# Kernel optimization log

Hardware: AMD Instinct MI355X
Metric: run time of the kernel (lower is better)

Reference implementation:

```python
import jax, jax.numpy as jnp
import numpy as np

B, T, F, H, L, C = 32, 512, 1024, 1024, 2, 2
W_SCALE = 0.03  # small init so tanh stays in its linear-ish range


def setup_inputs() -> dict:
    key = jax.random.key(0)
    ks = jax.random.split(key, 12)
    inp = {
        "x": jax.random.normal(ks[0], (B, T, F), dtype=jnp.float32),
        "h0": jax.random.normal(ks[1], (L, B, H), dtype=jnp.float32),
        # layer 0 (input size F)
        "W_ih0": jax.random.normal(ks[2], (H, F), dtype=jnp.float32) * W_SCALE,
        "W_hh0": jax.random.normal(ks[3], (H, H), dtype=jnp.float32) * W_SCALE,
        "b_ih0": jax.random.normal(ks[4], (H,), dtype=jnp.float32) * W_SCALE,
        "b_hh0": jax.random.normal(ks[5], (H,), dtype=jnp.float32) * W_SCALE,
        # layer 1 (input size H)
        "W_ih1": jax.random.normal(ks[6], (H, H), dtype=jnp.float32) * W_SCALE,
        "W_hh1": jax.random.normal(ks[7], (H, H), dtype=jnp.float32) * W_SCALE,
        "b_ih1": jax.random.normal(ks[8], (H,), dtype=jnp.float32) * W_SCALE,
        "b_hh1": jax.random.normal(ks[9], (H,), dtype=jnp.float32) * W_SCALE,
        # classifier Linear(T*H -> C)
        "W_cls": jax.random.normal(ks[10], (C, T * H), dtype=jnp.float32) * 0.001,
        "b_cls": jax.random.normal(ks[11], (C,), dtype=jnp.float32) * 0.001,
    }
    return inp


def _rnn_layer(x_btf, h0_bh, W_ih, W_hh, b_ih, b_hh):
    # PyTorch RNN (tanh): h_t = tanh(x_t W_ih^T + b_ih + h_{t-1} W_hh^T + b_hh)
    # Precompute the input projection for all timesteps (one big GEMM).
    pre = jnp.einsum("btf,hf->bth", x_btf, W_ih) + b_ih + b_hh  # [B,T,H]
    pre_t = jnp.swapaxes(pre, 0, 1)  # [T,B,H] for scan

    def step(h, p):  # h: [B,H], p: [B,H]
        h_new = jnp.tanh(p + h @ W_hh.T)
        return h_new, h_new

    h_last, ys = jax.lax.scan(step, h0_bh, pre_t)
    return jnp.swapaxes(ys, 0, 1), h_last  # [B,T,H], [B,H]


def reference(x, h0, W_ih0, W_hh0, b_ih0, b_hh0, W_ih1, W_hh1, b_ih1, b_hh1, W_cls, b_cls):
    y0, h0_last = _rnn_layer(x, h0[0], W_ih0, W_hh0, b_ih0, b_hh0)
    y1, h1_last = _rnn_layer(y0, h0[1], W_ih1, W_hh1, b_ih1, b_hh1)
    h_n = jnp.stack([h0_last, h1_last], axis=0)  # [L,B,H]
    flat = y1.reshape(y1.shape[0], -1)  # [B, T*H]
    logits = flat @ W_cls.T + b_cls  # Dropout(0.1) is identity at inference
    return logits, h_n
```

## Files before the change

kernel.cpp:

```cpp
#include <hip/hip_runtime.h>
#include <math.h>

typedef float f4 __attribute__((ext_vector_type(4)));
typedef short bf16x8 __attribute__((ext_vector_type(8)));
typedef unsigned u32x2 __attribute__((ext_vector_type(2)));
typedef unsigned u32x4 __attribute__((ext_vector_type(4)));

#define NT 512

#define H0R 0
#define H1R 131072
#define PLOG 196608
#define FLAGS 200704
#define WSW 204800
#define XBF 4399104

__device__ __forceinline__ unsigned pack_bf16(float lo, float hi) {
  unsigned u;
  asm volatile("v_cvt_pk_bf16_f32 %0, %1, %2" : "=v"(u) : "v"(lo), "v"(hi));
  return u;
}
__device__ __forceinline__ float bflo(unsigned d) { return __uint_as_float(d << 16); }
__device__ __forceinline__ float bfhi(unsigned d) { return __uint_as_float(d & 0xffff0000u); }
__device__ __forceinline__ void st_cohf(float* p, float v) {
  __hip_atomic_store(p, v, __ATOMIC_RELAXED, __HIP_MEMORY_SCOPE_AGENT);
}
__device__ __forceinline__ void st_cohu(unsigned* p, unsigned v) {
  __hip_atomic_store(p, v, __ATOMIC_RELAXED, __HIP_MEMORY_SCOPE_AGENT);
}
__device__ __forceinline__ int ld_flag(const unsigned* p) {
  return (int)__hip_atomic_load(p, __ATOMIC_RELAXED, __HIP_MEMORY_SCOPE_AGENT);
}

__device__ __forceinline__ void split8(const f4 v0, const f4 v1, u32x4& hi, u32x4& lo) {
  float h_[8] = {v0[0], v0[1], v0[2], v0[3], v1[0], v1[1], v1[2], v1[3]};
  #pragma unroll
  for (int e = 0; e < 4; ++e) hi[e] = pack_bf16(h_[2*e], h_[2*e+1]);
  float r[8];
  #pragma unroll
  for (int e = 0; e < 4; ++e) {
    r[2*e]   = h_[2*e]   - bflo(hi[e]);
    r[2*e+1] = h_[2*e+1] - bfhi(hi[e]);
  }
  #pragma unroll
  for (int e = 0; e < 4; ++e) lo[e] = pack_bf16(r[2*e], r[2*e+1]);
}

__global__ __launch_bounds__(128) void wconv_kernel(
    const float* __restrict__ W0, const float* __restrict__ W1,
    const float* __restrict__ W2, const float* __restrict__ W3,
    float* __restrict__ ws) {
  const int mat = blockIdx.x >> 10;
  const int j = blockIdx.x & 1023;
  const int kc = threadIdx.x;
  const float* Wm = (mat == 0) ? W0 : (mat == 1) ? W1 : (mat == 2) ? W2 : W3;
  const f4* src = (const f4*)(Wm + (size_t)j * 1024 + kc * 8);
  f4 v0 = src[0], v1 = src[1];
  u32x4 hi, lo;
  split8(v0, v1, hi, lo);
  u32x4* dst = (u32x4*)((f4*)ws + (WSW >> 2));
  size_t base = (size_t)(mat * 2) * 131072 + (j >> 4) * 2048 + kc * 16 + (j & 15);
  dst[base] = hi;
  dst[base + 131072] = lo;
}

__global__ __launch_bounds__(128) void xconv_kernel(const float* __restrict__ x,
                                                    float* __restrict__ ws) {
  const int t = blockIdx.x;
  const int kc = threadIdx.x;
  u32x4* dst = (u32x4*)((f4*)ws + (XBF >> 2)) + (size_t)t * 4096;
  for (int b = 0; b < 32; ++b) {
    const f4* src = (const f4*)(x + ((size_t)b * NT + t) * 1024 + kc * 8);
    f4 v0 = src[0], v1 = src[1];
    u32x4 p;
    #pragma unroll
    for (int e = 0; e < 4; ++e)
      p[e] = pack_bf16(e < 2 ? v0[2*e] : v1[2*e-4], e < 2 ? v0[2*e+1] : v1[2*e-3]);
    dst[(size_t)kc * 32 + b] = p;
  }
}

__global__ __launch_bounds__(256) void hinit_kernel(const float* __restrict__ h0,
                                                    float* __restrict__ ws) {
  int g = blockIdx.x * 256 + threadIdx.x;
  int l = g >> 12, b = (g >> 7) & 31, kc = g & 127;
  const f4* src = (const f4*)(h0 + (size_t)l * 32768 + b * 1024 + kc * 8);
  f4 v0 = src[0], v1 = src[1];
  u32x4 hi, lo;
  split8(v0, v1, hi, lo);
  unsigned base = l ? (H1R + 32768) : (H0R + 3 * 32768);
  u32x4* d = (u32x4*)((unsigned*)ws + base);
  d[(size_t)kc * 32 + b] = hi;
  d[4096 + (size_t)kc * 32 + b] = lo;
  if (g < 4096) ((unsigned*)ws)[FLAGS + g] = 0u;
}

#define LDG(dst, ptr) \
  asm volatile("global_load_dwordx4 %0, %1, off sc0" : "=v"(dst) : "v"(ptr))
#define MFMA(a, b, c) __builtin_amdgcn_mfma_f32_16x16x32_bf16(a, b, c, 0, 0, 0)
#define BC(v) __builtin_bit_cast(bf16x8, v)

#define KT_M(kt, N)                                                       \
  asm volatile("s_waitcnt vmcnt(" #N ")");                                \
  __builtin_amdgcn_sched_barrier(0xF4);                                   \
  {                                                                       \
    const int ci = (ch0 + kt * 4) * 16 + jl;                              \
    bf16x8 a0 = w4b[ci], a1 = w4b[2048 + ci];                             \
    bf16x8 vh = BC(bh[kt]), vl = BC(bl[kt]);                              \
    cr = MFMA(a0, vh, cr); cr = MFMA(a0, vl, cr); cr = MFMA(a1, vh, cr);  \
  }

#define KT_G(kt, N)                                                       \
  asm volatile("s_waitcnt vmcnt(" #N ")");                                \
  __builtin_amdgcn_sched_barrier(0xF4);                                   \
  {                                                                       \
    const int ci = (ch0 + kt * 4) * 16 + jl;                              \
    bf16x8 a2 = w4b[4096 + ci], a3 = w4b[6144 + ci];                      \
    bf16x8 vh = BC(gh[kt]), vl = BC(gl[kt]);                              \
    cp = MFMA(a2, vh, cp); cp = MFMA(a2, vl, cp); cp = MFMA(a3, vh, cp);  \
  }

#define KT_X(kt, N)                                                       \
  asm volatile("s_waitcnt vmcnt(" #N ")");                                \
  __builtin_amdgcn_sched_barrier(0xF4);                                   \
  {                                                                       \
    const int ci = (ch0 + kt * 4) * 16 + jl;                              \
    bf16x8 a2 = w4b[4096 + ci];                                           \
    cp = MFMA(a2, BC(bx[kt]), cp);                                        \
  }

#define LD16(A, B, pa, pb)                                                \
  LDG(A[0], pa);       LDG(B[0], pb);                                     \
  LDG(A[1], pa + 128); LDG(B[1], pb + 128);                               \
  LDG(A[2], pa + 256); LDG(B[2], pb + 256);                               \
  LDG(A[3], pa + 384); LDG(B[3], pb + 384);                               \
  LDG(A[4], pa + 512); LDG(B[4], pb + 512);                               \
  LDG(A[5], pa + 640); LDG(B[5], pb + 640);                               \
  LDG(A[6], pa + 768); LDG(B[6], pb + 768);                               \
  LDG(A[7], pa + 896); LDG(B[7], pb + 896);

__global__ __launch_bounds__(512, 1) void rnn_kernel(
    const float* __restrict__ bih0, const float* __restrict__ bhh0,
    const float* __restrict__ bih1, const float* __restrict__ bhh1,
    const float* __restrict__ Wcls, const float* __restrict__ bcls,
    float* __restrict__ out, float* ws) {
  extern __shared__ float smem[];
  f4* w4 = (f4*)smem;
  bf16x8* w4b = (bf16x8*)smem;
  f4* partR = w4 + 8192;
  f4* partP = w4 + 8704;
  float* prebuf = smem + 36864;

  const int bid = blockIdx.x, tid = threadIdx.x;
  const bool isL1 = bid >= 64;
  const int jsl = bid & 63;
  const int l = tid & 63, w = tid >> 6;
  const int nt = w & 1, ks = w >> 1;
  const int jl = l & 15;
  const int bcol = nt * 16 + (l & 15);
  const int ch0 = ks * 32 + (l >> 4);

  unsigned* flag0 = (unsigned*)ws + FLAGS;
  unsigned* flag1 = flag0 + 64 * 32;
  const f4* wsf4 = (const f4*)ws;

  {
    const int nent = isL1 ? 8192 : 6144;
    for (int i = tid; i < nent; i += 512) {
      const int slot = i >> 11, idx = i & 2047;
      const int region = isL1 ? (slot < 2 ? 6 + slot : 2 + slot) : slot;
      w4[i] = wsf4[(WSW >> 2) + (size_t)region * 131072 + jsl * 2048 + idx];
    }
  }

  const int rr = tid & 63, ntr = (tid >> 6) & 1;
  const int b_r = ntr * 16 + (rr & 15);
  const int jg = rr >> 4;
  const int jcol0 = jsl * 16 + jg * 4;
  f4 biasv = (f4)0.f;
  if (tid < 128) {
    f4 bi = isL1 ? *(const f4*)(bih1 + jcol0) : *(const f4*)(bih0 + jcol0);
    f4 bh2 = isL1 ? *(const f4*)(bhh1 + jcol0) : *(const f4*)(bhh0 + jcol0);
    biasv = bi + bh2;
  }
  float lg0 = 0.f, lg1 = 0.f;
  __syncthreads();

  if (!isL1) {
    f4 bx[8];
    const f4* px = wsf4 + (XBF >> 2) + ch0 * 32 + bcol;
    LDG(bx[0], px);       LDG(bx[1], px + 128);
    LDG(bx[2], px + 256); LDG(bx[3], px + 384);
    LDG(bx[4], px + 512); LDG(bx[5], px + 640);
    LDG(bx[6], px + 768); LDG(bx[7], px + 896);
    f4 cp = (f4)0.f;
    KT_X(0, 7) KT_X(1, 6) KT_X(2, 5) KT_X(3, 4)
    KT_X(4, 3) KT_X(5, 2) KT_X(6, 1) KT_X(7, 0)
    partP[(ks * 2 + nt) * 64 + l] = cp;
  } else {
    if (tid < 64) { while (ld_flag(&flag0[tid * 32]) < 1) {} }
    __syncthreads();
    __builtin_amdgcn_sched_barrier(0);
    const f4* gph = wsf4 + (H0R >> 2) + ch0 * 32 + bcol;
    const f4* gpl = gph + 4096;
    f4 gh[8], gl[8];
    LD16(gh, gl, gph, gpl)
    f4 cp = (f4)0.f;
    KT_G(0, 14) KT_G(1, 12) KT_G(2, 10) KT_G(3, 8)
    KT_G(4, 6)  KT_G(5, 4)  KT_G(6, 2)  KT_G(7, 0)
    partP[(ks * 2 + nt) * 64 + l] = cp;
  }
  __syncthreads();
  if (tid >= 128 && tid < 256) {
    f4 sum = partP[ntr * 64 + rr] + partP[(2 + ntr) * 64 + rr] +
             partP[(4 + ntr) * 64 + rr] + partP[(6 + ntr) * 64 + rr];
    #pragma unroll
    for (int e = 0; e < 4; ++e) prebuf[(jg * 4 + e) * 32 + b_r] = sum[e];
  }

  if (!isL1) {
    for (int s = 0; s < NT; ++s) {
      if (tid < 64) { while (ld_flag(&flag0[tid * 32]) < s) {} }
      else if (tid < 128) {
        const int bound = s - 3;
        while (ld_flag(&flag1[(tid - 64) * 32]) < bound) {}
      }
      __syncthreads();
      __builtin_amdgcn_sched_barrier(0);
      const int pp = s & 1;

      const f4* ph = wsf4 + (H0R >> 2) + ((s + 3) & 3) * 8192 + ch0 * 32 + bcol;
      const f4* pl = ph + 4096;
      f4 bh[8], bl[8];
      LD16(bh, bl, ph, pl)
      f4 cr = (f4)0.f;
      KT_M(0, 14) KT_M(1, 12) KT_M(2, 10) KT_M(3, 8)
      KT_M(4, 6)  KT_M(5, 4)  KT_M(6, 2)  KT_M(7, 0)
      partR[(ks * 2 + nt) * 64 + l] = cr;
      __syncthreads();

      if (tid < 128) {
        f4 sum = partR[ntr * 64 + rr] + partR[(2 + ntr) * 64 + rr] +
                 partR[(4 + ntr) * 64 + rr] + partR[(6 + ntr) * 64 + rr];
        float h_[4];
        #pragma unroll
        for (int e = 0; e < 4; ++e)
          h_[e] = tanhf(sum[e] + biasv[e] + prebuf[pp * 512 + (jg * 4 + e) * 32 + b_r]);
        unsigned hi0 = pack_bf16(h_[0], h_[1]), hi1 = pack_bf16(h_[2], h_[3]);
        unsigned lo0 = pack_bf16(h_[0] - bflo(hi0), h_[1] - bfhi(hi0));
        unsigned lo1 = pack_bf16(h_[2] - bflo(hi1), h_[3] - bfhi(hi1));
        u32x2 hp; hp[0] = hi0; hp[1] = hi1;
        u32x2 lp; lp[0] = lo0; lp[1] = lo1;
        unsigned* dp = (unsigned*)ws + H0R + (s & 3) * 32768 +
                       ((jcol0 >> 3) * 32 + b_r) * 4 + ((jcol0 >> 1) & 3);
        asm volatile("global_store_dwordx2 %0, %1, off sc0 sc1" ::"v"(dp), "v"(hp) : "memory");
        asm volatile("global_store_dwordx2 %0, %1, off sc0 sc1" ::"v"(dp + 16384), "v"(lp) : "memory");
        if (s == NT - 1) {
          f4 o; o[0]=h_[0]; o[1]=h_[1]; o[2]=h_[2]; o[3]=h_[3];
          *(f4*)(out + 64 + (size_t)b_r * 1024 + jcol0) = o;
        }
      }
      asm volatile("s_waitcnt vmcnt(0)");
      __syncthreads();
      if (tid == 0) st_cohu(&flag0[bid * 32], (unsigned)(s + 1));

      if (s < NT - 1) {
        const f4* px = wsf4 + (XBF >> 2) + (size_t)(s + 1) * 4096 + ch0 * 32 + bcol;
        f4 bx[8];
        LDG(bx[0], px);       LDG(bx[1], px + 128);
        LDG(bx[2], px + 256); LDG(bx[3], px + 384);
        LDG(bx[4], px + 512); LDG(bx[5], px + 640);
        LDG(bx[6], px + 768); LDG(bx[7], px + 896);
        f4 cp = (f4)0.f;
        KT_X(0, 7) KT_X(1, 6) KT_X(2, 5) KT_X(3, 4)
        KT_X(4, 3) KT_X(5, 2) KT_X(6, 1) KT_X(7, 0)
        partP[(ks * 2 + nt) * 64 + l] = cp;
        __syncthreads();
        if (tid >= 128 && tid < 256) {
          f4 sum = partP[ntr * 64 + rr] + partP[(2 + ntr) * 64 + rr] +
                   partP[(4 + ntr) * 64 + rr] + partP[(6 + ntr) * 64 + rr];
          #pragma unroll
          for (int e = 0; e < 4; ++e)
            prebuf[(pp ^ 1) * 512 + (jg * 4 + e) * 32 + b_r] = sum[e];
        }
      }
    }
  } else {
    for (int t = 0; t < NT; ++t) {
      if (tid < 64) { while (ld_flag(&flag1[tid * 32]) < t) {} }
      __syncthreads();
      __builtin_amdgcn_sched_barrier(0);
      const int pp = t & 1;

      f4 wc0 = (f4)0.f, wc1 = (f4)0.f;
      if (tid < 128) {
        wc0 = *(const f4*)(Wcls + (size_t)t * 1024 + jcol0);
        wc1 = *(const f4*)(Wcls + (size_t)524288 + (size_t)t * 1024 + jcol0);
      }
      __builtin_amdgcn_sched_barrier(0);

      const f4* ph = wsf4 + (H1R >> 2) + ((t + 1) & 1) * 8192 + ch0 * 32 + bcol;
      const f4* pl = ph + 4096;
      f4 bh[8], bl[8];
      LD16(bh, bl, ph, pl)
      f4 cr = (f4)0.f;
      KT_M(0, 14) KT_M(1, 12) KT_M(2, 10) KT_M(3, 8)
      KT_M(4, 6)  KT_M(5, 4)  KT_M(6, 2)  KT_M(7, 0)
      partR[(ks * 2 + nt) * 64 + l] = cr;
      __syncthreads();

      if (tid < 128) {
        f4 sum = partR[ntr * 64 + rr] + partR[(2 + ntr) * 64 + rr] +
                 partR[(4 + ntr) * 64 + rr] + partR[(6 + ntr) * 64 + rr];
        float h_[4];
        #pragma unroll
        for (int e = 0; e < 4; ++e)
          h_[e] = tanhf(sum[e] + biasv[e] + prebuf[pp * 512 + (jg * 4 + e) * 32 + b_r]);
        unsigned hi0 = pack_bf16(h_[0], h_[1]), hi1 = pack_bf16(h_[2], h_[3]);
        unsigned lo0 = pack_bf16(h_[0] - bflo(hi0), h_[1] - bfhi(hi0));
        unsigned lo1 = pack_bf16(h_[2] - bflo(hi1), h_[3] - bfhi(hi1));
        u32x2 hp; hp[0] = hi0; hp[1] = hi1;
        u32x2 lp; lp[0] = lo0; lp[1] = lo1;
        unsigned* dp = (unsigned*)ws + H1R + (t & 1) * 32768 +
                       ((jcol0 >> 3) * 32 + b_r) * 4 + ((jcol0 >> 1) & 3);
        asm volatile("global_store_dwordx2 %0, %1, off sc0 sc1" ::"v"(dp), "v"(hp) : "memory");
        asm volatile("global_store_dwordx2 %0, %1, off sc0 sc1" ::"v"(dp + 16384), "v"(lp) : "memory");
        lg0 += h_[0]*wc0[0] + h_[1]*wc0[1] + h_[2]*wc0[2] + h_[3]*wc0[3];
        lg1 += h_[0]*wc1[0] + h_[1]*wc1[1] + h_[2]*wc1[2] + h_[3]*wc1[3];
        if (t == NT - 1) {
          f4 o; o[0]=h_[0]; o[1]=h_[1]; o[2]=h_[2]; o[3]=h_[3];
          *(f4*)(out + 64 + 32768 + (size_t)b_r * 1024 + jcol0) = o;
        }
      }
      asm volatile("s_waitcnt vmcnt(0)");
      __syncthreads();
      if (tid == 0) st_cohu(&flag1[(bid - 64) * 32], (unsigned)(t + 1));

      if (t < NT - 1) {
        if (tid < 64) { while (ld_flag(&flag0[tid * 32]) < t + 2) {} }
        __syncthreads();
        __builtin_amdgcn_sched_barrier(0);
        const f4* gph = wsf4 + (H0R >> 2) + ((t + 1) & 3) * 8192 + ch0 * 32 + bcol;
        const f4* gpl = gph + 4096;
        f4 gh[8], gl[8];
        LD16(gh, gl, gph, gpl)
        f4 cp = (f4)0.f;
        KT_G(0, 14) KT_G(1, 12) KT_G(2, 10) KT_G(3, 8)
        KT_G(4, 6)  KT_G(5, 4)  KT_G(6, 2)  KT_G(7, 0)
        partP[(ks * 2 + nt) * 64 + l] = cp;
        __syncthreads();
        if (tid >= 128 && tid < 256) {
          f4 sum = partP[ntr * 64 + rr] + partP[(2 + ntr) * 64 + rr] +
                   partP[(4 + ntr) * 64 + rr] + partP[(6 + ntr) * 64 + rr];
          #pragma unroll
          for (int e = 0; e < 4; ++e)
            prebuf[(pp ^ 1) * 512 + (jg * 4 + e) * 32 + b_r] = sum[e];
        }
      }
    }
    float* lgred = (float*)(w4 + 8192);
    __syncthreads();
    if (tid < 128) {
      lgred[jg * 32 + b_r] = lg0;
      lgred[128 + jg * 32 + b_r] = lg1;
    }
    __syncthreads();
    if (tid < 64) {
      const int c = tid >> 5, bb = tid & 31;
      float v = 0.f;
      #pragma unroll
      for (int g2 = 0; g2 < 4; ++g2) v += lgred[c * 128 + g2 * 32 + bb];
      st_cohf(&ws[PLOG + (size_t)(bid - 64) * 64 + c * 32 + bb], v);
    }
    __syncthreads();
    if (tid == 0) st_cohu(&flag1[(bid - 64) * 32], 600u);
  }

  if (bid == 0) {
    if (tid < 64) { while (ld_flag(&flag1[tid * 32]) < 600) {} }
    __syncthreads();
    __builtin_amdgcn_sched_barrier(0);
    float* lgred = (float*)(w4 + 8192);
    if (tid < 256) {
      const int g2 = tid >> 6, pair = tid & 63;
      float v = 0.f;
      for (int blk = g2; blk < 64; blk += 4)
        v += __hip_atomic_load(&ws[PLOG + (size_t)blk * 64 + pair],
                               __ATOMIC_RELAXED, __HIP_MEMORY_SCOPE_AGENT);
      lgred[tid] = v;
    }
    __syncthreads();
    if (tid < 64) {
      float s2 = bcls[tid >> 5];
      #pragma unroll
      for (int g2 = 0; g2 < 4; ++g2) s2 += lgred[g2 * 64 + tid];
      out[(size_t)(tid & 31) * 2 + (tid >> 5)] = s2;
    }
  }
}

extern "C" void kernel_launch(void* const* d_in, const int* in_sizes, int n_in,
                              void* d_out, int out_size, void* d_ws, size_t ws_size,
                              hipStream_t stream) {
  const float* x    = (const float*)d_in[0];
  const float* h0   = (const float*)d_in[1];
  const float* Wih0 = (const float*)d_in[2];
  const float* Whh0 = (const float*)d_in[3];
  const float* bih0 = (const float*)d_in[4];
  const float* bhh0 = (const float*)d_in[5];
  const float* Wih1 = (const float*)d_in[6];
  const float* Whh1 = (const float*)d_in[7];
  const float* bih1 = (const float*)d_in[8];
  const float* bhh1 = (const float*)d_in[9];
  const float* Wcls = (const float*)d_in[10];
  const float* bcls = (const float*)d_in[11];
  float* out = (float*)d_out;
  float* ws  = (float*)d_ws;

  hipFuncSetAttribute((const void*)rnn_kernel,
                      hipFuncAttributeMaxDynamicSharedMemorySize, 151552);

  hipLaunchKernelGGL(wconv_kernel, dim3(4096), dim3(128), 0, stream,
                     Whh0, Wih0, Wih1, Whh1, ws);
  hipLaunchKernelGGL(xconv_kernel, dim3(512), dim3(128), 0, stream, x, ws);
  hipLaunchKernelGGL(hinit_kernel, dim3(32), dim3(256), 0, stream, h0, ws);

  void* args[] = { (void*)&bih0, (void*)&bhh0, (void*)&bih1, (void*)&bhh1,
                   (void*)&Wcls, (void*)&bcls, (void*)&out, (void*)&ws };
  hipLaunchCooperativeKernel((void*)rnn_kernel, dim3(128), dim3(512), args,
                             151552, stream);
}
```

Baseline: 2.417 ms.

## Restructure persistent RNN into warp-specialized recurrence and projection waves with per-warp flags

Cuts the block to 256 threads and gives each wave the full K reduction, so the cross-wave partial-sum reduction through shared memory is gone. Two waves run the recurrent step while the other two compute the next step's input projection at the same time. Per-wave flags are read with 64-bit loads, one per pair of waves. Loads now run as a deeper 16-deep pipelined MFMA stream. The risk is higher register pressure (32 f4 buffers) and a longer serial K-chain per wave on the critical path.

New measurement: 2.778 ms. +14.9%, slower.

```diff
diff --git a/kernel.cpp b/kernel.cpp
--- a/kernel.cpp
+++ b/kernel.cpp
@@ -28,8 +28,8 @@
 __device__ __forceinline__ void st_cohu(unsigned* p, unsigned v) {
   __hip_atomic_store(p, v, __ATOMIC_RELAXED, __HIP_MEMORY_SCOPE_AGENT);
 }
-__device__ __forceinline__ int ld_flag(const unsigned* p) {
-  return (int)__hip_atomic_load(p, __ATOMIC_RELAXED, __HIP_MEMORY_SCOPE_AGENT);
+__device__ __forceinline__ unsigned long long ld64(const unsigned long long* p) {
+  return __hip_atomic_load(p, __ATOMIC_RELAXED, __HIP_MEMORY_SCOPE_AGENT);
 }
 
 __device__ __forceinline__ void split8(const f4 v0, const f4 v1, u32x4& hi, u32x4& lo) {
@@ -97,49 +97,68 @@
 
 #define LDG(dst, ptr) \
   asm volatile("global_load_dwordx4 %0, %1, off sc0" : "=v"(dst) : "v"(ptr))
+#define LDP(dst, ptr) \
+  asm volatile("global_load_dwordx4 %0, %1, off" : "=v"(dst) : "v"(ptr))
+#define STG2(ptr, val) \
+  asm volatile("global_store_dwordx2 %0, %1, off sc0 sc1" ::"v"(ptr), "v"(val) : "memory")
 #define MFMA(a, b, c) __builtin_amdgcn_mfma_f32_16x16x32_bf16(a, b, c, 0, 0, 0)
 #define BC(v) __builtin_bit_cast(bf16x8, v)
 
-#define KT_M(kt, N)                                                       \
+#define ISSM(p) LDG(bh[(p) & 15], ph + (p) * 128); LDG(bl[(p) & 15], pl + (p) * 128);
+#define ISS_A ISSM(0) ISSM(1) ISSM(2) ISSM(3) ISSM(4) ISSM(5) ISSM(6) ISSM(7) \
+  ISSM(8) ISSM(9) ISSM(10) ISSM(11) ISSM(12) ISSM(13) ISSM(14) ISSM(15)
+
+#define KT_M(m, N)                                                        \
   asm volatile("s_waitcnt vmcnt(" #N ")");                                \
   __builtin_amdgcn_sched_barrier(0xF4);                                   \
   {                                                                       \
-    const int ci = (ch0 + kt * 4) * 16 + jl;                              \
+    const int ci = ((kg + (m) * 4) << 4) + jl;                            \
     bf16x8 a0 = w4b[ci], a1 = w4b[2048 + ci];                             \
-    bf16x8 vh = BC(bh[kt]), vl = BC(bl[kt]);                              \
+    bf16x8 vh = BC(bh[(m) & 15]), vl = BC(bl[(m) & 15]);                  \
     cr = MFMA(a0, vh, cr); cr = MFMA(a0, vl, cr); cr = MFMA(a1, vh, cr);  \
   }
-
-#define KT_G(kt, N)                                                       \
+#define KT_G(m, N)                                                        \
   asm volatile("s_waitcnt vmcnt(" #N ")");                                \
   __builtin_amdgcn_sched_barrier(0xF4);                                   \
   {                                                                       \
-    const int ci = (ch0 + kt * 4) * 16 + jl;                              \
+    const int ci = ((kg + (m) * 4) << 4) + jl;                            \
     bf16x8 a2 = w4b[4096 + ci], a3 = w4b[6144 + ci];                      \
-    bf16x8 vh = BC(gh[kt]), vl = BC(gl[kt]);                              \
+    bf16x8 vh = BC(bh[(m) & 15]), vl = BC(bl[(m) & 15]);                  \
     cp = MFMA(a2, vh, cp); cp = MFMA(a2, vl, cp); cp = MFMA(a3, vh, cp);  \
   }
-
-#define KT_X(kt, N)                                                       \
+#define KT_X(m, N)                                                        \
   asm volatile("s_waitcnt vmcnt(" #N ")");                                \
   __builtin_amdgcn_sched_barrier(0xF4);                                   \
   {                                                                       \
-    const int ci = (ch0 + kt * 4) * 16 + jl;                              \
+    const int ci = ((kg + (m) * 4) << 4) + jl;                            \
     bf16x8 a2 = w4b[4096 + ci];                                           \
-    cp = MFMA(a2, BC(bx[kt]), cp);                                        \
-  }
-
-#define LD16(A, B, pa, pb)                                                \
-  LDG(A[0], pa);       LDG(B[0], pb);                                     \
-  LDG(A[1], pa + 128); LDG(B[1], pb + 128);                               \
-  LDG(A[2], pa + 256); LDG(B[2], pb + 256);                               \
-  LDG(A[3], pa + 384); LDG(B[3], pb + 384);                               \
-  LDG(A[4], pa + 512); LDG(B[4], pb + 512);                               \
-  LDG(A[5], pa + 640); LDG(B[5], pb + 640);                               \
-  LDG(A[6], pa + 768); LDG(B[6], pb + 768);                               \
-  LDG(A[7], pa + 896); LDG(B[7], pb + 896);
-
-__global__ __launch_bounds__(512, 1) void rnn_kernel(
+    cp = MFMA(a2, BC(bx[m]), cp);                                         \
+  }
+
+#define PIPE(KT)                                                          \
+  ISS_A                                                                   \
+  KT(0,30)  ISSM(16) KT(1,30)  ISSM(17) KT(2,30)  ISSM(18) KT(3,30)  ISSM(19) \
+  KT(4,30)  ISSM(20) KT(5,30)  ISSM(21) KT(6,30)  ISSM(22) KT(7,30)  ISSM(23) \
+  KT(8,30)  ISSM(24) KT(9,30)  ISSM(25) KT(10,30) ISSM(26) KT(11,30) ISSM(27) \
+  KT(12,30) ISSM(28) KT(13,30) ISSM(29) KT(14,30) ISSM(30) KT(15,30) ISSM(31) \
+  KT(16,30) KT(17,28) KT(18,26) KT(19,24) KT(20,22) KT(21,20) KT(22,18)   \
+  KT(23,16) KT(24,14) KT(25,12) KT(26,10) KT(27,8) KT(28,6) KT(29,4)      \
+  KT(30,2)  KT(31,0)
+
+#define REP32(F) F(0) F(1) F(2) F(3) F(4) F(5) F(6) F(7) F(8) F(9) F(10) F(11) \
+  F(12) F(13) F(14) F(15) F(16) F(17) F(18) F(19) F(20) F(21) F(22) F(23) \
+  F(24) F(25) F(26) F(27) F(28) F(29) F(30) F(31)
+#define LDXM(m) LDP(bx[m], px + (m) * 128);
+#define KTXLIST(KT) KT(0,31) KT(1,30) KT(2,29) KT(3,28) KT(4,27) KT(5,26) \
+  KT(6,25) KT(7,24) KT(8,23) KT(9,22) KT(10,21) KT(11,20) KT(12,19) KT(13,18) \
+  KT(14,17) KT(15,16) KT(16,15) KT(17,14) KT(18,13) KT(19,12) KT(20,11) \
+  KT(21,10) KT(22,9) KT(23,8) KT(24,7) KT(25,6) KT(26,5) KT(27,4) KT(28,3) \
+  KT(29,2) KT(30,1) KT(31,0)
+
+#define F0L(lx) ((const unsigned long long*)(flg + (lx) * 32))
+#define F1L(lx) ((const unsigned long long*)(flg + 2048 + (lx) * 32))
+
+__global__ __launch_bounds__(256, 1) void rnn_kernel(
     const float* __restrict__ bih0, const float* __restrict__ bhh0,
     const float* __restrict__ bih1, const float* __restrict__ bhh1,
     const float* __restrict__ Wcls, const float* __restrict__ bcls,
@@ -147,38 +166,32 @@
   extern __shared__ float smem[];
   f4* w4 = (f4*)smem;
   bf16x8* w4b = (bf16x8*)smem;
-  f4* partR = w4 + 8192;
-  f4* partP = w4 + 8704;
-  float* prebuf = smem + 36864;
+  float* prebuf = smem + 32768;
+  float* lgred = prebuf;
 
   const int bid = blockIdx.x, tid = threadIdx.x;
   const bool isL1 = bid >= 64;
   const int jsl = bid & 63;
-  const int l = tid & 63, w = tid >> 6;
-  const int nt = w & 1, ks = w >> 1;
-  const int jl = l & 15;
-  const int bcol = nt * 16 + (l & 15);
-  const int ch0 = ks * 32 + (l >> 4);
-
-  unsigned* flag0 = (unsigned*)ws + FLAGS;
-  unsigned* flag1 = flag0 + 64 * 32;
+  const int w = tid >> 6, l = tid & 63;
+  const int jl = l & 15, kg = l >> 4;
+  const int nt = w & 1;
+  const int bcol = nt * 16 + jl;
+  const int j0 = kg * 4;
+  const int jcol0 = jsl * 16 + j0;
+
+  unsigned* flg = (unsigned*)ws + FLAGS;
   const f4* wsf4 = (const f4*)ws;
 
   {
     const int nent = isL1 ? 8192 : 6144;
-    for (int i = tid; i < nent; i += 512) {
+    for (int i = tid; i < nent; i += 256) {
       const int slot = i >> 11, idx = i & 2047;
       const int region = isL1 ? (slot < 2 ? 6 + slot : 2 + slot) : slot;
       w4[i] = wsf4[(WSW >> 2) + (size_t)region * 131072 + jsl * 2048 + idx];
     }
   }
-
-  const int rr = tid & 63, ntr = (tid >> 6) & 1;
-  const int b_r = ntr * 16 + (rr & 15);
-  const int jg = rr >> 4;
-  const int jcol0 = jsl * 16 + jg * 4;
   f4 biasv = (f4)0.f;
-  if (tid < 128) {
+  if (w < 2) {
     f4 bi = isL1 ? *(const f4*)(bih1 + jcol0) : *(const f4*)(bih0 + jcol0);
     f4 bh2 = isL1 ? *(const f4*)(bhh1 + jcol0) : *(const f4*)(bhh0 + jcol0);
     biasv = bi + bh2;
@@ -187,214 +200,174 @@
   __syncthreads();
 
   if (!isL1) {
-    f4 bx[8];
-    const f4* px = wsf4 + (XBF >> 2) + ch0 * 32 + bcol;
-    LDG(bx[0], px);       LDG(bx[1], px + 128);
-    LDG(bx[2], px + 256); LDG(bx[3], px + 384);
-    LDG(bx[4], px + 512); LDG(bx[5], px + 640);
-    LDG(bx[6], px + 768); LDG(bx[7], px + 896);
-    f4 cp = (f4)0.f;
-    KT_X(0, 7) KT_X(1, 6) KT_X(2, 5) KT_X(3, 4)
-    KT_X(4, 3) KT_X(5, 2) KT_X(6, 1) KT_X(7, 0)
-    partP[(ks * 2 + nt) * 64 + l] = cp;
-  } else {
-    if (tid < 64) { while (ld_flag(&flag0[tid * 32]) < 1) {} }
-    __syncthreads();
-    __builtin_amdgcn_sched_barrier(0);
-    const f4* gph = wsf4 + (H0R >> 2) + ch0 * 32 + bcol;
-    const f4* gpl = gph + 4096;
-    f4 gh[8], gl[8];
-    LD16(gh, gl, gph, gpl)
-    f4 cp = (f4)0.f;
-    KT_G(0, 14) KT_G(1, 12) KT_G(2, 10) KT_G(3, 8)
-    KT_G(4, 6)  KT_G(5, 4)  KT_G(6, 2)  KT_G(7, 0)
-    partP[(ks * 2 + nt) * 64 + l] = cp;
-  }
-  __syncthreads();
-  if (tid >= 128 && tid < 256) {
-    f4 sum = partP[ntr * 64 + rr] + partP[(2 + ntr) * 64 + rr] +
-             partP[(4 + ntr) * 64 + rr] + partP[(6 + ntr) * 64 + rr];
-    #pragma unroll
-    for (int e = 0; e < 4; ++e) prebuf[(jg * 4 + e) * 32 + b_r] = sum[e];
-  }
-
-  if (!isL1) {
-    for (int s = 0; s < NT; ++s) {
-      if (tid < 64) { while (ld_flag(&flag0[tid * 32]) < s) {} }
-      else if (tid < 128) {
-        const int bound = s - 3;
-        while (ld_flag(&flag1[(tid - 64) * 32]) < bound) {}
+    for (int s = -1; s < NT; ++s) {
+      if (w < 2) {
+        if (s >= 0) {
+          {
+            const unsigned long long* p0 = F0L(l);
+            const unsigned long long* p1 = F1L(l);
+            const int b1 = s - 3;
+            while (true) {
+              unsigned long long v0 = ld64(p0);
+              unsigned long long v1 = ld64(p1);
+              if ((int)(unsigned)v0 >= s && (int)(unsigned)(v0 >> 32) >= s &&
+                  (int)(unsigned)v1 >= b1 && (int)(unsigned)(v1 >> 32) >= b1)
+                break;
+            }
+          }
+          __builtin_amdgcn_sched_barrier(0);
+          const f4* ph = wsf4 + ((s + 3) & 3) * 8192 + kg * 32 + bcol;
+          const f4* pl = ph + 4096;
+          f4 bh[16], bl[16];
+          f4 cr = (f4)0.f;
+          PIPE(KT_M)
+          const int pp = s & 1;
+          float h_[4];
+          #pragma unroll
+          for (int e = 0; e < 4; ++e)
+            h_[e] = tanhf(cr[e] + biasv[e] +
+                          prebuf[pp * 528 + (j0 + e) * 33 + bcol]);
+          unsigned hi0 = pack_bf16(h_[0], h_[1]), hi1 = pack_bf16(h_[2], h_[3]);
+          unsigned lo0 = pack_bf16(h_[0] - bflo(hi0), h_[1] - bfhi(hi0));
+          unsigned lo1 = pack_bf16(h_[2] - bflo(hi1), h_[3] - bfhi(hi1));
+          u32x2 hp; hp[0] = hi0; hp[1] = hi1;
+          u32x2 lp; lp[0] = lo0; lp[1] = lo1;
+          unsigned* dp = (unsigned*)ws + H0R + (s & 3) * 32768 +
+                         ((jcol0 >> 3) * 32 + bcol) * 4 + ((jcol0 >> 1) & 3);
+          STG2(dp, hp);
+          STG2(dp + 16384, lp);
+          if (s == NT - 1) {
+            f4 o; o[0] = h_[0]; o[1] = h_[1]; o[2] = h_[2]; o[3] = h_[3];
+            *(f4*)(out + 64 + (size_t)bcol * 1024 + jcol0) = o;
+          }
+          asm volatile("s_waitcnt vmcnt(0)" ::: "memory");
+          st_cohu(&flg[bid * 32 + w], (unsigned)(s + 1));
+        }
+      } else {
+        if (s < NT - 1) {
+          const f4* px = wsf4 + (XBF >> 2) + (size_t)(s + 1) * 4096 +
+                         kg * 32 + bcol;
+          f4 bx[32];
+          f4 cp = (f4)0.f;
+          REP32(LDXM)
+          KTXLIST(KT_X)
+          const int ppn = (s + 1) & 1;
+          #pragma unroll
+          for (int e = 0; e < 4; ++e)
+            prebuf[ppn * 528 + (j0 + e) * 33 + bcol] = cp[e];
+        }
+      }
+      __syncthreads();
+    }
+    if (bid == 0) {
+      if (tid < 64) {
+        const unsigned long long* p1 = F1L(tid);
+        while (true) {
+          unsigned long long v = ld64(p1);
+          if ((unsigned)v >= 600u && (unsigned)(v >> 32) >= 600u) break;
+        }
       }
       __syncthreads();
       __builtin_amdgcn_sched_barrier(0);
-      const int pp = s & 1;
-
-      const f4* ph = wsf4 + (H0R >> 2) + ((s + 3) & 3) * 8192 + ch0 * 32 + bcol;
-      const f4* pl = ph + 4096;
-      f4 bh[8], bl[8];
-      LD16(bh, bl, ph, pl)
-      f4 cr = (f4)0.f;
-      KT_M(0, 14) KT_M(1, 12) KT_M(2, 10) KT_M(3, 8)
-      KT_M(4, 6)  KT_M(5, 4)  KT_M(6, 2)  KT_M(7, 0)
-      partR[(ks * 2 + nt) * 64 + l] = cr;
+      {
+        const int g2 = tid >> 6, pair = tid & 63;
+        float v = 0.f;
+        for (int blk = g2; blk < 64; blk += 4)
+          v += __hip_atomic_load(&ws[PLOG + (size_t)blk * 64 + pair],
+                                 __ATOMIC_RELAXED, __HIP_MEMORY_SCOPE_AGENT);
+        lgred[tid] = v;
+      }
       __syncthreads();
-
-      if (tid < 128) {
-        f4 sum = partR[ntr * 64 + rr] + partR[(2 + ntr) * 64 + rr] +
-                 partR[(4 + ntr) * 64 + rr] + partR[(6 + ntr) * 64 + rr];
-        float h_[4];
+      if (tid < 64) {
+        float s2 = bcls[tid >> 5];
         #pragma unroll
-        for (int e = 0; e < 4; ++e)
-          h_[e] = tanhf(sum[e] + biasv[e] + prebuf[pp * 512 + (jg * 4 + e) * 32 + b_r]);
-        unsigned hi0 = pack_bf16(h_[0], h_[1]), hi1 = pack_bf16(h_[2], h_[3]);
-        unsigned lo0 = pack_bf16(h_[0] - bflo(hi0), h_[1] - bfhi(hi0));
-        unsigned lo1 = pack_bf16(h_[2] - bflo(hi1), h_[3] - bfhi(hi1));
-        u32x2 hp; hp[0] = hi0; hp[1] = hi1;
-        u32x2 lp; lp[0] = lo0; lp[1] = lo1;
-        unsigned* dp = (unsigned*)ws + H0R + (s & 3) * 32768 +
-                       ((jcol0 >> 3) * 32 + b_r) * 4 + ((jcol0 >> 1) & 3);
-        asm volatile("global_store_dwordx2 %0, %1, off sc0 sc1" ::"v"(dp), "v"(hp) : "memory");
-        asm volatile("global_store_dwordx2 %0, %1, off sc0 sc1" ::"v"(dp + 16384), "v"(lp) : "memory");
-        if (s == NT - 1) {
-          f4 o; o[0]=h_[0]; o[1]=h_[1]; o[2]=h_[2]; o[3]=h_[3];
-          *(f4*)(out + 64 + (size_t)b_r * 1024 + jcol0) = o;
+        for (int g2 = 0; g2 < 4; ++g2) s2 += lgred[g2 * 64 + tid];
+        out[(size_t)(tid & 31) * 2 + (tid >> 5)] = s2;
+      }
+    }
+  } else {
+    for (int t = -1; t < NT; ++t) {
+      if (w < 2) {
+        if (t >= 0) {
+          {
+            const unsigned long long* p1 = F1L(l);
+            while (true) {
+              unsigned long long v = ld64(p1);
+              if ((int)(unsigned)v >= t && (int)(unsigned)(v >> 32) >= t) break;
+            }
+          }
+          __builtin_amdgcn_sched_barrier(0);
+          f4 wc0 = *(const f4*)(Wcls + (size_t)t * 1024 + jcol0);
+          f4 wc1 = *(const f4*)(Wcls + 524288 + (size_t)t * 1024 + jcol0);
+          __builtin_amdgcn_sched_barrier(0);
+          const f4* ph = wsf4 + (H1R >> 2) + ((t + 1) & 1) * 8192 +
+                         kg * 32 + bcol;
+          const f4* pl = ph + 4096;
+          f4 bh[16], bl[16];
+          f4 cr = (f4)0.f;
+          PIPE(KT_M)
+          const int pp = t & 1;
+          float h_[4];
+          #pragma unroll
+          for (int e = 0; e < 4; ++e)
+            h_[e] = tanhf(cr[e] + biasv[e] +
+                          prebuf[pp * 528 + (j0 + e) * 33 + bcol]);
+          unsigned hi0 = pack_bf16(h_[0], h_[1]), hi1 = pack_bf16(h_[2], h_[3]);
+          unsigned lo0 = pack_bf16(h_[0] - bflo(hi0), h_[1] - bfhi(hi0));
+          unsigned lo1 = pack_bf16(h_[2] - bflo(hi1), h_[3] - bfhi(hi1));
+          u32x2 hp; hp[0] = hi0; hp[1] = hi1;
+          u32x2 lp; lp[0] = lo0; lp[1] = lo1;
+          unsigned* dp = (unsigned*)ws + H1R + (t & 1) * 32768 +
+                         ((jcol0 >> 3) * 32 + bcol) * 4 + ((jcol0 >> 1) & 3);
+          STG2(dp, hp);
+          STG2(dp + 16384, lp);
+          if (t == NT - 1) {
+            f4 o; o[0] = h_[0]; o[1] = h_[1]; o[2] = h_[2]; o[3] = h_[3];
+            *(f4*)(out + 64 + 32768 + (size_t)bcol * 1024 + jcol0) = o;
+          }
+          lg0 += h_[0]*wc0[0] + h_[1]*wc0[1] + h_[2]*wc0[2] + h_[3]*wc0[3];
+          lg1 += h_[0]*wc1[0] + h_[1]*wc1[1] + h_[2]*wc1[2] + h_[3]*wc1[3];
+          asm volatile("s_waitcnt vmcnt(0)" ::: "memory");
+          st_cohu(&flg[2048 + (bid - 64) * 32 + w], (unsigned)(t + 1));
+        }
+      } else {
+        if (t < NT - 1) {
+          {
+            const unsigned long long* p0 = F0L(l);
+            const int b0 = t + 2;
+            while (true) {
+              unsigned long long v = ld64(p0);
+              if ((int)(unsigned)v >= b0 && (int)(unsigned)(v >> 32) >= b0) break;
+            }
+          }
+          __builtin_amdgcn_sched_barrier(0);
+          const f4* ph = wsf4 + ((t + 1) & 3) * 8192 + kg * 32 + bcol;
+          const f4* pl = ph + 4096;
+          f4 bh[16], bl[16];
+          f4 cp = (f4)0.f;
+          PIPE(KT_G)
+          const int ppn = (t + 1) & 1;
+          #pragma unroll
+          for (int e = 0; e < 4; ++e)
+            prebuf[ppn * 528 + (j0 + e) * 33 + bcol] = cp[e];
         }
       }
-      asm volatile("s_waitcnt vmcnt(0)");
       __syncthreads();
-      if (tid == 0) st_cohu(&flag0[bid * 32], (unsigned)(s + 1));
-
-      if (s < NT - 1) {
-        const f4* px = wsf4 + (XBF >> 2) + (size_t)(s + 1) * 4096 + ch0 * 32 + bcol;
-        f4 bx[8];
-        LDG(bx[0], px);       LDG(bx[1], px + 128);
-        LDG(bx[2], px + 256); LDG(bx[3], px + 384);
-        LDG(bx[4], px + 512); LDG(bx[5], px + 640);
-        LDG(bx[6], px + 768); LDG(bx[7], px + 896);
-        f4 cp = (f4)0.f;
-        KT_X(0, 7) KT_X(1, 6) KT_X(2, 5) KT_X(3, 4)
-        KT_X(4, 3) KT_X(5, 2) KT_X(6, 1) KT_X(7, 0)
-        partP[(ks * 2 + nt) * 64 + l] = cp;
-        __syncthreads();
-        if (tid >= 128 && tid < 256) {
-          f4 sum = partP[ntr * 64 + rr] + partP[(2 + ntr) * 64 + rr] +
-                   partP[(4 + ntr) * 64 + rr] + partP[(6 + ntr) * 64 + rr];
-          #pragma unroll
-          for (int e = 0; e < 4; ++e)
-            prebuf[(pp ^ 1) * 512 + (jg * 4 + e) * 32 + b_r] = sum[e];
-        }
-      }
-    }
-  } else {
-    for (int t = 0; t < NT; ++t) {
-      if (tid < 64) { while (ld_flag(&flag1[tid * 32]) < t) {} }
-      __syncthreads();
-      __builtin_amdgcn_sched_barrier(0);
-      const int pp = t & 1;
-
-      f4 wc0 = (f4)0.f, wc1 = (f4)0.f;
-      if (tid < 128) {
-        wc0 = *(const f4*)(Wcls + (size_t)t * 1024 + jcol0);
-        wc1 = *(const f4*)(Wcls + (size_t)524288 + (size_t)t * 1024 + jcol0);
-      }
-      __builtin_amdgcn_sched_barrier(0);
-
-      const f4* ph = wsf4 + (H1R >> 2) + ((t + 1) & 1) * 8192 + ch0 * 32 + bcol;
-      const f4* pl = ph + 4096;
-      f4 bh[8], bl[8];
-      LD16(bh, bl, ph, pl)
-      f4 cr = (f4)0.f;
-      KT_M(0, 14) KT_M(1, 12) KT_M(2, 10) KT_M(3, 8)
-      KT_M(4, 6)  KT_M(5, 4)  KT_M(6, 2)  KT_M(7, 0)
-      partR[(ks * 2 + nt) * 64 + l] = cr;
-      __syncthreads();
-
-      if (tid < 128) {
-        f4 sum = partR[ntr * 64 + rr] + partR[(2 + ntr) * 64 + rr] +
-                 partR[(4 + ntr) * 64 + rr] + partR[(6 + ntr) * 64 + rr];
-        float h_[4];
-        #pragma unroll
-        for (int e = 0; e < 4; ++e)
-          h_[e] = tanhf(sum[e] + biasv[e] + prebuf[pp * 512 + (jg * 4 + e) * 32 + b_r]);
-        unsigned hi0 = pack_bf16(h_[0], h_[1]), hi1 = pack_bf16(h_[2], h_[3]);
-        unsigned lo0 = pack_bf16(h_[0] - bflo(hi0), h_[1] - bfhi(hi0));
-        unsigned lo1 = pack_bf16(h_[2] - bflo(hi1), h_[3] - bfhi(hi1));
-        u32x2 hp; hp[0] = hi0; hp[1] = hi1;
-        u32x2 lp; lp[0] = lo0; lp[1] = lo1;
-        unsigned* dp = (unsigned*)ws + H1R + (t & 1) * 32768 +
-                       ((jcol0 >> 3) * 32 + b_r) * 4 + ((jcol0 >> 1) & 3);
-        asm volatile("global_store_dwordx2 %0, %1, off sc0 sc1" ::"v"(dp), "v"(hp) : "memory");
-        asm volatile("global_store_dwordx2 %0, %1, off sc0 sc1" ::"v"(dp + 16384), "v"(lp) : "memory");
-        lg0 += h_[0]*wc0[0] + h_[1]*wc0[1] + h_[2]*wc0[2] + h_[3]*wc0[3];
-        lg1 += h_[0]*wc1[0] + h_[1]*wc1[1] + h_[2]*wc1[2] + h_[3]*wc1[3];
-        if (t == NT - 1) {
-          f4 o; o[0]=h_[0]; o[1]=h_[1]; o[2]=h_[2]; o[3]=h_[3];
-          *(f4*)(out + 64 + 32768 + (size_t)b_r * 1024 + jcol0) = o;
-        }
-      }
-      asm volatile("s_waitcnt vmcnt(0)");
-      __syncthreads();
-      if (tid == 0) st_cohu(&flag1[(bid - 64) * 32], (unsigned)(t + 1));
-
-      if (t < NT - 1) {
-        if (tid < 64) { while (ld_flag(&flag0[tid * 32]) < t + 2) {} }
-        __syncthreads();
-        __builtin_amdgcn_sched_barrier(0);
-        const f4* gph = wsf4 + (H0R >> 2) + ((t + 1) & 3) * 8192 + ch0 * 32 + bcol;
-        const f4* gpl = gph + 4096;
-        f4 gh[8], gl[8];
-        LD16(gh, gl, gph, gpl)
-        f4 cp = (f4)0.f;
-        KT_G(0, 14) KT_G(1, 12) KT_G(2, 10) KT_G(3, 8)
-        KT_G(4, 6)  KT_G(5, 4)  KT_G(6, 2)  KT_G(7, 0)
-        partP[(ks * 2 + nt) * 64 + l] = cp;
-        __syncthreads();
-        if (tid >= 128 && tid < 256) {
-          f4 sum = partP[ntr * 64 + rr] + partP[(2 + ntr) * 64 + rr] +
-                   partP[(4 + ntr) * 64 + rr] + partP[(6 + ntr) * 64 + rr];
-          #pragma unroll
-          for (int e = 0; e < 4; ++e)
-            prebuf[(pp ^ 1) * 512 + (jg * 4 + e) * 32 + b_r] = sum[e];
-        }
-      }
-    }
-    float* lgred = (float*)(w4 + 8192);
-    __syncthreads();
-    if (tid < 128) {
-      lgred[jg * 32 + b_r] = lg0;
-      lgred[128 + jg * 32 + b_r] = lg1;
+    }
+    if (w < 2) {
+      lg0 += __shfl_xor(lg0, 16); lg0 += __shfl_xor(lg0, 32);
+      lg1 += __shfl_xor(lg1, 16); lg1 += __shfl_xor(lg1, 32);
+      if (kg == 0) { lgred[bcol] = lg0; lgred[32 + bcol] = lg1; }
     }
     __syncthreads();
     if (tid < 64) {
-      const int c = tid >> 5, bb = tid & 31;
-      float v = 0.f;
-      #pragma unroll
-      for (int g2 = 0; g2 < 4; ++g2) v += lgred[c * 128 + g2 * 32 + bb];
-      st_cohf(&ws[PLOG + (size_t)(bid - 64) * 64 + c * 32 + bb], v);
+      st_cohf(&ws[PLOG + (size_t)(bid - 64) * 64 + tid], lgred[tid]);
+      asm volatile("s_waitcnt vmcnt(0)" ::: "memory");
     }
     __syncthreads();
-    if (tid == 0) st_cohu(&flag1[(bid - 64) * 32], 600u);
-  }
-
-  if (bid == 0) {
-    if (tid < 64) { while (ld_flag(&flag1[tid * 32]) < 600) {} }
-    __syncthreads();
-    __builtin_amdgcn_sched_barrier(0);
-    float* lgred = (float*)(w4 + 8192);
-    if (tid < 256) {
-      const int g2 = tid >> 6, pair = tid & 63;
-      float v = 0.f;
-      for (int blk = g2; blk < 64; blk += 4)
-        v += __hip_atomic_load(&ws[PLOG + (size_t)blk * 64 + pair],
-                               __ATOMIC_RELAXED, __HIP_MEMORY_SCOPE_AGENT);
-      lgred[tid] = v;
-    }
-    __syncthreads();
-    if (tid < 64) {
-      float s2 = bcls[tid >> 5];
-      #pragma unroll
-      for (int g2 = 0; g2 < 4; ++g2) s2 += lgred[g2 * 64 + tid];
-      out[(size_t)(tid & 31) * 2 + (tid >> 5)] = s2;
+    if (tid == 0) {
+      st_cohu(&flg[2048 + (bid - 64) * 32 + 0], 600u);
+      st_cohu(&flg[2048 + (bid - 64) * 32 + 1], 600u);
     }
   }
 }
@@ -418,7 +391,7 @@
   float* ws  = (float*)d_ws;
 
   hipFuncSetAttribute((const void*)rnn_kernel,
-                      hipFuncAttributeMaxDynamicSharedMemorySize, 151552);
+                      hipFuncAttributeMaxDynamicSharedMemorySize, 135296);
 
   hipLaunchKernelGGL(wconv_kernel, dim3(4096), dim3(128), 0, stream,
                      Whh0, Wih0, Wih1, Whh1, ws);
@@ -427,6 +400,10 @@
 
   void* args[] = { (void*)&bih0, (void*)&bhh0, (void*)&bih1, (void*)&bhh1,
                    (void*)&Wcls, (void*)&bcls, (void*)&out, (void*)&ws };
-  hipLaunchCooperativeKernel((void*)rnn_kernel, dim3(128), dim3(512), args,
-                             151552, stream);
-}
+  hipError_t e = hipLaunchCooperativeKernel((void*)rnn_kernel, dim3(128),
+                                            dim3(256), args, 135296, stream);
+  if (e != hipSuccess) {
+    hipLaunchKernelGGL(rnn_kernel, dim3(128), dim3(256), 135296, stream,
+                       bih0, bhh0, bih1, bhh1, Wcls, bcls, out, ws);
+  }
+}
```
